# Kernel tuning notes

Measured on AMD Instinct MI355X. Metric: run time of the kernel, lower is better.

The kernel has to match this reference:

```python
import jax, jax.numpy as jnp
import numpy as np
from jax import lax

B, QL, N_IN, H = 64, 2048, 256, 64


def setup_inputs() -> dict:
    key = jax.random.key(0)
    ks = jax.random.split(key, 8)
    s = 1.0 / np.sqrt(H)  # PyTorch LSTMCell init scale
    return {
        "h_concat": jax.random.normal(ks[0], (B, QL, N_IN), dtype=jnp.float32),
        "w21": jax.random.normal(ks[1], (N_IN, 1), dtype=jnp.float32),
        "w22": jax.random.normal(ks[2], (H, 1), dtype=jnp.float32),
        "bias2": jax.random.normal(ks[3], (1,), dtype=jnp.float32),
        "W_ih": jax.random.uniform(ks[4], (4 * H, N_IN + 1), dtype=jnp.float32, minval=-s, maxval=s),
        "W_hh": jax.random.uniform(ks[5], (4 * H, H), dtype=jnp.float32, minval=-s, maxval=s),
        "b_ih": jax.random.uniform(ks[6], (4 * H,), dtype=jnp.float32, minval=-s, maxval=s),
        "b_hh": jax.random.uniform(ks[7], (4 * H,), dtype=jnp.float32, minval=-s, maxval=s),
    }


def reference(h_concat, w21, w22, bias2, W_ih, W_hh, b_ih, b_hh):
    Bsz, T, n_in = h_concat.shape
    nh = W_hh.shape[1]

    def step(carry, x):
        h, c = carry  # [B,H] each; x: [B,n_in]
        # sigmoid gate: pz_t = sigmoid(x @ w21 + h @ w22 + bias2) -> [B,1]
        pz = jax.nn.sigmoid(x @ w21 + h @ w22 + bias2)
        hz = jnp.concatenate([x, pz], axis=1)  # [B, n_in+1]
        # LSTMCell (PyTorch gate order: i, f, g, o)
        gates = hz @ W_ih.T + b_ih + h @ W_hh.T + b_hh  # [B,4H]
        i, f, g, o = jnp.split(gates, 4, axis=1)
        c_new = jax.nn.sigmoid(f) * c + jax.nn.sigmoid(i) * jnp.tanh(g)
        h_new = jax.nn.sigmoid(o) * jnp.tanh(c_new)
        return (h_new, c_new), pz[:, 0]

    h0 = jnp.zeros((Bsz, nh), dtype=h_concat.dtype)
    c0 = jnp.zeros((Bsz, nh), dtype=h_concat.dtype)
    xs = jnp.swapaxes(h_concat, 0, 1)  # [T,B,n_in]
    _, Z = lax.scan(step, (h0, c0), xs)  # Z: [T,B]
    return jnp.swapaxes(Z, 0, 1)  # [B,T]
```

## Files before the change

kernel.cpp:

```cpp
#include <hip/hip_runtime.h>

#define TT 2048
#define BB 64

typedef _Float16 v2h __attribute__((ext_vector_type(2)));

__device__ __forceinline__ float frcp(float x) { return __builtin_amdgcn_rcpf(x); }
__device__ __forceinline__ float fsig(float x) { return frcp(1.f + __expf(-x)); }
__device__ __forceinline__ float ftan(float x) { return 1.f - 2.f * frcp(1.f + __expf(2.f * x)); }

#if __has_builtin(__builtin_amdgcn_fdot2)
#define FDOT2(a, b, c) __builtin_amdgcn_fdot2((a), (b), (c), false)
#else
#define FDOT2(a, b, c) ((c) + (float)(a).x * (float)(b).x + (float)(a).y * (float)(b).y)
#endif

#define DPPADD(x, ctrl)                                                        \
  (x) += __builtin_bit_cast(float, __builtin_amdgcn_update_dpp(                \
             0, __builtin_bit_cast(int, (x)), (ctrl), 0xf, 0xf, true))

__device__ __forceinline__ float wave_sum64(float x) {
  DPPADD(x, 0x111);
  DPPADD(x, 0x112);
  DPPADD(x, 0x114);
  DPPADD(x, 0x118);
  DPPADD(x, 0x142);
  DPPADD(x, 0x143);
  return __builtin_bit_cast(
      float, __builtin_amdgcn_readlane(__builtin_bit_cast(int, x), 63));
}

__global__ __launch_bounds__(256) void gates_gemm(const float* __restrict__ X,
                                                  const float* __restrict__ W,
                                                  const float* __restrict__ bih,
                                                  const float* __restrict__ bhh,
                                                  float* __restrict__ G,
                                                  int t0, int Tc) {
  __shared__ __align__(16) float As[32][64];
  __shared__ __align__(16) float Bs[32][64];
  const int tid = threadIdx.x;
  const int m0 = blockIdx.x * 64;
  const int n0 = blockIdx.y * 64;
  const int bb = m0 / Tc;
  const int tt0 = m0 - bb * Tc;
  const int tx = tid & 15, ty = tid >> 4;
  const int r  = tid >> 2;
  const int kq = (tid & 3) * 8;
  const float* xrow = X + ((size_t)(bb * TT + t0 + tt0 + r)) * 256 + kq;
  const float* wrow = W + (size_t)(n0 + r) * 257 + kq;
  float acc[4][4] = {};
  for (int k0 = 0; k0 < 256; k0 += 32) {
    float4 a0 = *reinterpret_cast<const float4*>(xrow + k0);
    float4 a1 = *reinterpret_cast<const float4*>(xrow + k0 + 4);
    float bv[8];
#pragma unroll
    for (int u = 0; u < 8; ++u) bv[u] = wrow[k0 + u];
    if (k0 != 0) __syncthreads();
    As[kq+0][r]=a0.x; As[kq+1][r]=a0.y; As[kq+2][r]=a0.z; As[kq+3][r]=a0.w;
    As[kq+4][r]=a1.x; As[kq+5][r]=a1.y; As[kq+6][r]=a1.z; As[kq+7][r]=a1.w;
#pragma unroll
    for (int u = 0; u < 8; ++u) Bs[kq+u][r] = bv[u];
    __syncthreads();
#pragma unroll
    for (int kk = 0; kk < 32; ++kk) {
      float4 av = *reinterpret_cast<const float4*>(&As[kk][ty*4]);
      float4 bw = *reinterpret_cast<const float4*>(&Bs[kk][tx*4]);
      const float aa[4] = {av.x, av.y, av.z, av.w};
      const float bbv[4] = {bw.x, bw.y, bw.z, bw.w};
#pragma unroll
      for (int i = 0; i < 4; ++i)
#pragma unroll
        for (int j = 0; j < 4; ++j) acc[i][j] += aa[i] * bbv[j];
    }
  }
  const int col = n0 + tx * 4;
  float bsum[4];
#pragma unroll
  for (int j = 0; j < 4; ++j) bsum[j] = bih[col + j] + bhh[col + j];
#pragma unroll
  for (int i = 0; i < 4; ++i) {
    float4 o;
    o.x = acc[i][0] + bsum[0];
    o.y = acc[i][1] + bsum[1];
    o.z = acc[i][2] + bsum[2];
    o.w = acc[i][3] + bsum[3];
    *reinterpret_cast<float4*>(&G[(size_t)(m0 + ty*4 + i) * 256 + col]) = o;
  }
}

__global__ __launch_bounds__(256) void pz_kernel(const float* __restrict__ X,
                                                 const float* __restrict__ w21,
                                                 const float* __restrict__ bias2,
                                                 float* __restrict__ P,
                                                 int t0, int Tc) {
  const int r = blockIdx.x * 4 + (threadIdx.x >> 6);
  const int lane = threadIdx.x & 63;
  const int bb = r / Tc;
  const int tt = r - bb * Tc;
  const float4 xv = *reinterpret_cast<const float4*>(
      &X[((size_t)(bb * TT + t0 + tt)) * 256 + lane * 4]);
  const float4 wv = *reinterpret_cast<const float4*>(&w21[lane * 4]);
  float s = xv.x*wv.x + xv.y*wv.y + xv.z*wv.z + xv.w*wv.w;
#pragma unroll
  for (int o = 32; o; o >>= 1) s += __shfl_xor(s, o);
  if (lane == 0) P[r] = s + bias2[0];
}

__global__ __launch_bounds__(64, 1) void lstm_seq7(
    const float* __restrict__ G, const float* __restrict__ P,
    const float* __restrict__ Wih, const float* __restrict__ Whh,
    const float* __restrict__ w22, float* __restrict__ Z,
    float* __restrict__ hq, float* __restrict__ cq, int t0, int Tc) {
  const int l = threadIdx.x;
  const int b = blockIdx.x;
  __shared__ __align__(16) _Float16 hsm[64];

  v2h wh[4][32];
#pragma unroll
  for (int q = 0; q < 4; ++q) {
#pragma unroll
    for (int j = 0; j < 16; ++j) {
      float4 v = *reinterpret_cast<const float4*>(&Whh[(size_t)(q*64 + l)*64 + 4*j]);
      v2h pA, pB;
      pA.x = (_Float16)v.x; pA.y = (_Float16)v.y;
      pB.x = (_Float16)v.z; pB.y = (_Float16)v.w;
      wh[q][2*j] = pA; wh[q][2*j+1] = pB;
    }
  }
  float wihL[4];
#pragma unroll
  for (int q = 0; q < 4; ++q) wihL[q] = Wih[(size_t)(q*64 + l)*257 + 256];
  const float w22r = w22[l];

  float h = 0.f, c = 0.f;
  if (t0 != 0) { h = hq[b * 64 + l]; c = cq[b * 64 + l]; }
  hsm[l] = (_Float16)h;
  __builtin_amdgcn_wave_barrier();

  const float* Gb = G + (size_t)b * Tc * 256 + l;
  const float* Pb = P + (size_t)b * Tc;
  float* Zb = Z + (size_t)b * TT + t0;

  float gr[4][4], pr[4];
#pragma unroll
  for (int u = 0; u < 4; ++u) {
    const float* Gt = Gb + (size_t)u * 256;
#pragma unroll
    for (int q = 0; q < 4; ++q) gr[u][q] = Gt[q * 64];
    pr[u] = Pb[u];
  }

  for (int tt = 0; tt < Tc; tt += 4) {
    float zs[4];
#pragma unroll
    for (int uu = 0; uu < 4; ++uu) {
      const int step = tt + uu;
      const float gx0 = gr[uu][0], gx1 = gr[uu][1];
      const float gx2 = gr[uu][2], gx3 = gr[uu][3];
      const float p0 = pr[uu];
      int pf = step + 4; if (pf > Tc - 1) pf = Tc - 1;
      {
        const float* Gt = Gb + (size_t)pf * 256;
#pragma unroll
        for (int q = 0; q < 4; ++q) gr[uu][q] = Gt[q * 64];
        pr[uu] = Pb[pf];
      }

      const float tot = wave_sum64(h * w22r);
      const float pz = fsig(tot + p0);

      float d0a=0.f,d0b=0.f,d1a=0.f,d1b=0.f,d2a=0.f,d2b=0.f,d3a=0.f,d3b=0.f;
      const uint4* hp = reinterpret_cast<const uint4*>(hsm);
#pragma unroll
      for (int jj = 0; jj < 8; ++jj) {
        const uint4 uq = hp[jj];
        const v2h ha = __builtin_bit_cast(v2h, uq.x);
        const v2h hb = __builtin_bit_cast(v2h, uq.y);
        const v2h hc = __builtin_bit_cast(v2h, uq.z);
        const v2h hd = __builtin_bit_cast(v2h, uq.w);
        d0a = FDOT2(ha, wh[0][4*jj+0], d0a); d0b = FDOT2(hb, wh[0][4*jj+1], d0b);
        d0a = FDOT2(hc, wh[0][4*jj+2], d0a); d0b = FDOT2(hd, wh[0][4*jj+3], d0b);
        d1a = FDOT2(ha, wh[1][4*jj+0], d1a); d1b = FDOT2(hb, wh[1][4*jj+1], d1b);
        d1a = FDOT2(hc, wh[1][4*jj+2], d1a); d1b = FDOT2(hd, wh[1][4*jj+3], d1b);
        d2a = FDOT2(ha, wh[2][4*jj+0], d2a); d2b = FDOT2(hb, wh[2][4*jj+1], d2b);
        d2a = FDOT2(hc, wh[2][4*jj+2], d2a); d2b = FDOT2(hd, wh[2][4*jj+3], d2b);
        d3a = FDOT2(ha, wh[3][4*jj+0], d3a); d3b = FDOT2(hb, wh[3][4*jj+1], d3b);
        d3a = FDOT2(hc, wh[3][4*jj+2], d3a); d3b = FDOT2(hd, wh[3][4*jj+3], d3b);
      }
      const float pre0 = gx0 + pz * wihL[0] + (d0a + d0b);
      const float pre1 = gx1 + pz * wihL[1] + (d1a + d1b);
      const float pre2 = gx2 + pz * wihL[2] + (d2a + d2b);
      const float pre3 = gx3 + pz * wihL[3] + (d3a + d3b);

      const float ai = fsig(pre0);
      const float af = fsig(pre1);
      const float ag = ftan(pre2);
      const float ao = fsig(pre3);
      c = af * c + ai * ag;
      h = ao * ftan(c);

      __builtin_amdgcn_wave_barrier();
      hsm[l] = (_Float16)h;
      __builtin_amdgcn_wave_barrier();
      zs[uu] = pz;
    }
    if (l == 0) {
      float4 zo; zo.x = zs[0]; zo.y = zs[1]; zo.z = zs[2]; zo.w = zs[3];
      *reinterpret_cast<float4*>(&Zb[tt]) = zo;
    }
  }
  hq[b * 64 + l] = h;
  cq[b * 64 + l] = c;
}

__global__ __launch_bounds__(256) void lstm_fallback(const float* __restrict__ X,
    const float* __restrict__ w21, const float* __restrict__ w22,
    const float* __restrict__ bias2, const float* __restrict__ Wih,
    const float* __restrict__ Whh, const float* __restrict__ bih,
    const float* __restrict__ bhh, float* __restrict__ Z) {
  const int b = blockIdx.x;
  const int g = threadIdx.x;
  const int lane = g & 63;
  __shared__ __align__(16) float h_s[64];
  __shared__ float act_s[256];
  __shared__ __align__(16) float x_s[256];
  __shared__ __align__(16) float w21_s[256];
  float wh[64];
#pragma unroll
  for (int j = 0; j < 64; j += 4) {
    float4 v = *reinterpret_cast<const float4*>(&Whh[(size_t)g*64 + j]);
    wh[j]=v.x; wh[j+1]=v.y; wh[j+2]=v.z; wh[j+3]=v.w;
  }
  const float wihL = Wih[(size_t)g*257 + 256];
  const float bias = bih[g] + bhh[g];
  const float b2 = bias2[0];
  const float w22r = w22[lane];
  w21_s[g] = w21[g];
  if (g < 64) h_s[g] = 0.f;
  float c = 0.f;
  __syncthreads();
  const float* Wr = Wih + (size_t)g * 257;
  for (int t = 0; t < TT; ++t) {
    x_s[g] = X[((size_t)b*TT + t)*256 + g];
    __syncthreads();
    float pv = h_s[lane] * w22r;
    {
      const float4 xq = *reinterpret_cast<const float4*>(&x_s[lane*4]);
      const float4 wq = *reinterpret_cast<const float4*>(&w21_s[lane*4]);
      pv += xq.x*wq.x + xq.y*wq.y + xq.z*wq.z + xq.w*wq.w;
    }
#pragma unroll
    for (int o = 32; o; o >>= 1) pv += __shfl_xor(pv, o);
    const float pz = fsig(pv + b2);
    float a0=0.f, a1=0.f, a2=0.f, a3=0.f;
#pragma unroll
    for (int j = 0; j < 64; j += 4) {
      float4 hv = *reinterpret_cast<const float4*>(&h_s[j]);
      a0 += hv.x*wh[j]; a1 += hv.y*wh[j+1]; a2 += hv.z*wh[j+2]; a3 += hv.w*wh[j+3];
    }
    float xd0=0.f, xd1=0.f, xd2=0.f, xd3=0.f;
    for (int k = 0; k < 256; k += 4) {
      const float4 xq = *reinterpret_cast<const float4*>(&x_s[k]);
      xd0 += xq.x*Wr[k]; xd1 += xq.y*Wr[k+1]; xd2 += xq.z*Wr[k+2]; xd3 += xq.w*Wr[k+3];
    }
    const float pre = bias + pz*wihL + ((a0+a1)+(a2+a3)) + ((xd0+xd1)+(xd2+xd3));
    act_s[g] = ((g >> 6) == 2) ? ftan(pre) : fsig(pre);
    if (g == 0) Z[(size_t)b*TT + t] = pz;
    __syncthreads();
    if (g < 64) {
      const float iv = act_s[g], fv = act_s[64+g], gv = act_s[128+g], ov = act_s[192+g];
      c = fv*c + iv*gv;
      h_s[g] = ov * ftan(c);
    }
    __syncthreads();
  }
}

extern "C" void kernel_launch(void* const* d_in, const int* in_sizes, int n_in,
                              void* d_out, int out_size, void* d_ws, size_t ws_size,
                              hipStream_t stream) {
  const float* X     = (const float*)d_in[0];
  const float* w21   = (const float*)d_in[1];
  const float* w22   = (const float*)d_in[2];
  const float* bias2 = (const float*)d_in[3];
  const float* Wih   = (const float*)d_in[4];
  const float* Whh   = (const float*)d_in[5];
  const float* bih   = (const float*)d_in[6];
  const float* bhh   = (const float*)d_in[7];
  float* Z = (float*)d_out;

  int Tc = 0;
  for (int cand = 2048; cand >= 64; cand >>= 1) {
    size_t need = (size_t)cand * (64*256*4 + 64*4) + 2*64*64*4;
    if (ws_size >= need) { Tc = cand; break; }
  }
  if (Tc == 0) {
    lstm_fallback<<<dim3(64), dim3(256), 0, stream>>>(X, w21, w22, bias2, Wih, Whh, bih, bhh, Z);
    return;
  }
  float* Gbuf = (float*)d_ws;
  float* Pbuf = Gbuf + (size_t)64 * Tc * 256;
  float* hq   = Pbuf + (size_t)64 * Tc;
  float* cq   = hq + 64 * 64;
  for (int t0 = 0; t0 < 2048; t0 += Tc) {
    gates_gemm<<<dim3(Tc, 4), dim3(256), 0, stream>>>(X, Wih, bih, bhh, Gbuf, t0, Tc);
    pz_kernel<<<dim3(16 * Tc), dim3(256), 0, stream>>>(X, w21, bias2, Pbuf, t0, Tc);
    lstm_seq7<<<dim3(BB), dim3(64), 0, stream>>>(
        Gbuf, Pbuf, Wih, Whh, w22, Z, hq, cq, t0, Tc);
  }
}
```

Before: 1.194 ms.

## Use fp16 MFMA for input-gate GEMM with 64x128 tiles

Replaces the scalar FP32 tiled GEMM that precomputes input-projection gates with a kernel using 16x16x16 fp16 MFMA instructions. Inputs and weights are converted to half precision when staged into shared memory, and each block now covers 128 output columns, halving the grid's y dimension. This offloads the large non-recurrent GEMM to matrix cores, at the cost of fp16 rounding of X and W_ih. The sequential LSTM kernel is unchanged and may dominate total time.

```diff
diff --git a/kernel.cpp b/kernel.cpp
--- a/kernel.cpp
+++ b/kernel.cpp
@@ -4,6 +4,8 @@
 #define BB 64
 
 typedef _Float16 v2h __attribute__((ext_vector_type(2)));
+typedef _Float16 v4h __attribute__((ext_vector_type(4)));
+typedef float v4f __attribute__((ext_vector_type(4)));
 
 __device__ __forceinline__ float frcp(float x) { return __builtin_amdgcn_rcpf(x); }
 __device__ __forceinline__ float fsig(float x) { return frcp(1.f + __expf(-x)); }
@@ -30,61 +32,79 @@
       float, __builtin_amdgcn_readlane(__builtin_bit_cast(int, x), 63));
 }
 
-__global__ __launch_bounds__(256) void gates_gemm(const float* __restrict__ X,
-                                                  const float* __restrict__ W,
-                                                  const float* __restrict__ bih,
-                                                  const float* __restrict__ bhh,
-                                                  float* __restrict__ G,
-                                                  int t0, int Tc) {
-  __shared__ __align__(16) float As[32][64];
-  __shared__ __align__(16) float Bs[32][64];
+__global__ __launch_bounds__(256) void gates_gemm_mfma(
+    const float* __restrict__ X, const float* __restrict__ W,
+    const float* __restrict__ bih, const float* __restrict__ bhh,
+    float* __restrict__ G, int t0, int Tc) {
+  __shared__ __align__(16) _Float16 Xs[64][40];
+  __shared__ __align__(16) _Float16 Ws[128][40];
   const int tid = threadIdx.x;
   const int m0 = blockIdx.x * 64;
-  const int n0 = blockIdx.y * 64;
+  const int n0 = blockIdx.y * 128;
   const int bb = m0 / Tc;
   const int tt0 = m0 - bb * Tc;
-  const int tx = tid & 15, ty = tid >> 4;
-  const int r  = tid >> 2;
-  const int kq = (tid & 3) * 8;
-  const float* xrow = X + ((size_t)(bb * TT + t0 + tt0 + r)) * 256 + kq;
-  const float* wrow = W + (size_t)(n0 + r) * 257 + kq;
-  float acc[4][4] = {};
+  const int w = tid >> 6, l = tid & 63;
+  const int lr = l & 15, lk = l >> 4;
+
+  const int srow = tid >> 2, skq = (tid & 3) * 8;
+  const int wri = tid >> 1, wkh = (tid & 1) * 16;
+  const float* xrow = X + (size_t)(bb * TT + t0 + tt0 + srow) * 256 + skq;
+  const float* wrow = W + (size_t)(n0 + wri) * 257 + wkh;
+
+  float bsum[8];
+#pragma unroll
+  for (int nf = 0; nf < 8; ++nf)
+    bsum[nf] = bih[n0 + nf * 16 + lr] + bhh[n0 + nf * 16 + lr];
+
+  v4f acc[8];
+#pragma unroll
+  for (int nf = 0; nf < 8; ++nf) acc[nf] = (v4f){0.f, 0.f, 0.f, 0.f};
+
   for (int k0 = 0; k0 < 256; k0 += 32) {
-    float4 a0 = *reinterpret_cast<const float4*>(xrow + k0);
-    float4 a1 = *reinterpret_cast<const float4*>(xrow + k0 + 4);
-    float bv[8];
-#pragma unroll
-    for (int u = 0; u < 8; ++u) bv[u] = wrow[k0 + u];
+    float xa[8], wa[16];
+#pragma unroll
+    for (int u = 0; u < 8; ++u) xa[u] = xrow[k0 + u];
+#pragma unroll
+    for (int u = 0; u < 16; ++u) wa[u] = wrow[k0 + u];
     if (k0 != 0) __syncthreads();
-    As[kq+0][r]=a0.x; As[kq+1][r]=a0.y; As[kq+2][r]=a0.z; As[kq+3][r]=a0.w;
-    As[kq+4][r]=a1.x; As[kq+5][r]=a1.y; As[kq+6][r]=a1.z; As[kq+7][r]=a1.w;
-#pragma unroll
-    for (int u = 0; u < 8; ++u) Bs[kq+u][r] = bv[u];
+    {
+      uint xw[4];
+#pragma unroll
+      for (int u = 0; u < 4; ++u) {
+        v2h p; p.x = (_Float16)xa[2*u]; p.y = (_Float16)xa[2*u+1];
+        xw[u] = __builtin_bit_cast(uint, p);
+      }
+      *reinterpret_cast<uint4*>(&Xs[srow][skq]) =
+          make_uint4(xw[0], xw[1], xw[2], xw[3]);
+      uint ww[8];
+#pragma unroll
+      for (int u = 0; u < 8; ++u) {
+        v2h p; p.x = (_Float16)wa[2*u]; p.y = (_Float16)wa[2*u+1];
+        ww[u] = __builtin_bit_cast(uint, p);
+      }
+      *reinterpret_cast<uint4*>(&Ws[wri][wkh]) =
+          make_uint4(ww[0], ww[1], ww[2], ww[3]);
+      *reinterpret_cast<uint4*>(&Ws[wri][wkh + 8]) =
+          make_uint4(ww[4], ww[5], ww[6], ww[7]);
+    }
     __syncthreads();
-#pragma unroll
-    for (int kk = 0; kk < 32; ++kk) {
-      float4 av = *reinterpret_cast<const float4*>(&As[kk][ty*4]);
-      float4 bw = *reinterpret_cast<const float4*>(&Bs[kk][tx*4]);
-      const float aa[4] = {av.x, av.y, av.z, av.w};
-      const float bbv[4] = {bw.x, bw.y, bw.z, bw.w};
-#pragma unroll
-      for (int i = 0; i < 4; ++i)
-#pragma unroll
-        for (int j = 0; j < 4; ++j) acc[i][j] += aa[i] * bbv[j];
-    }
-  }
-  const int col = n0 + tx * 4;
-  float bsum[4];
-#pragma unroll
-  for (int j = 0; j < 4; ++j) bsum[j] = bih[col + j] + bhh[col + j];
-#pragma unroll
-  for (int i = 0; i < 4; ++i) {
-    float4 o;
-    o.x = acc[i][0] + bsum[0];
-    o.y = acc[i][1] + bsum[1];
-    o.z = acc[i][2] + bsum[2];
-    o.w = acc[i][3] + bsum[3];
-    *reinterpret_cast<float4*>(&G[(size_t)(m0 + ty*4 + i) * 256 + col]) = o;
+    const v4h a0 = *reinterpret_cast<const v4h*>(&Xs[w * 16 + lr][lk * 4]);
+    const v4h a1 = *reinterpret_cast<const v4h*>(&Xs[w * 16 + lr][16 + lk * 4]);
+#pragma unroll
+    for (int nf = 0; nf < 8; ++nf) {
+      const v4h b0 = *reinterpret_cast<const v4h*>(&Ws[nf * 16 + lr][lk * 4]);
+      const v4h b1 = *reinterpret_cast<const v4h*>(&Ws[nf * 16 + lr][16 + lk * 4]);
+      acc[nf] = __builtin_amdgcn_mfma_f32_16x16x16f16(a0, b0, acc[nf], 0, 0, 0);
+      acc[nf] = __builtin_amdgcn_mfma_f32_16x16x16f16(a1, b1, acc[nf], 0, 0, 0);
+    }
+  }
+  const int grow = m0 + w * 16 + lk * 4;
+#pragma unroll
+  for (int nf = 0; nf < 8; ++nf) {
+#pragma unroll
+    for (int j = 0; j < 4; ++j) {
+      G[(size_t)(grow + j) * 256 + n0 + nf * 16 + lr] = acc[nf][j] + bsum[nf];
+    }
   }
 }
 
@@ -303,7 +323,8 @@
   float* hq   = Pbuf + (size_t)64 * Tc;
   float* cq   = hq + 64 * 64;
   for (int t0 = 0; t0 < 2048; t0 += Tc) {
-    gates_gemm<<<dim3(Tc, 4), dim3(256), 0, stream>>>(X, Wih, bih, bhh, Gbuf, t0, Tc);
+    gates_gemm_mfma<<<dim3(Tc, 2), dim3(256), 0, stream>>>(X, Wih, bih, bhh,
+                                                           Gbuf, t0, Tc);
     pz_kernel<<<dim3(16 * Tc), dim3(256), 0, stream>>>(X, w21, bias2, Pbuf, t0, Tc);
     lstm_seq7<<<dim3(BB), dim3(64), 0, stream>>>(
         Gbuf, Pbuf, Wih, Whh, w22, Z, hq, cq, t0, Tc);
```

Result: faster. 1.049 ms (-12.1%).
